# Performance work log

Measured on AMD Instinct MI355X. Metric: run time of the kernel, lower is better.

## Reference

```python
import jax, jax.numpy as jnp
import numpy as np

N_NODES = 50000
N_EDGES = 800000
DIM = 128
HEADS = 2
DEPTH = 2
MLP = 512
NEG_SLOPE = 0.2  # PyG GATv2 default
EPS = 1e-5


def setup_inputs() -> dict:
    key = jax.random.key(0)
    ks = jax.random.split(key, 10)
    s = 0.05
    p = lambda k, shape: (jax.random.normal(k, shape, jnp.float32) * s)
    x = jax.random.normal(ks[0], (N_NODES, DIM), jnp.float32)
    edge_index = jax.random.randint(ks[1], (2, N_EDGES), 0, N_NODES, dtype=jnp.int64)
    D, H = DEPTH, HEADS
    return {
        "x": x,
        "edge_index": edge_index,
        # per-layer stacked params (leading dim = depth)
        "ln1_g": jnp.ones((D, DIM), jnp.float32), "ln1_b": jnp.zeros((D, DIM), jnp.float32),
        "Wl": p(ks[2], (D, DIM, H * DIM)), "bl": jnp.zeros((D, H * DIM), jnp.float32),
        "Wr": p(ks[3], (D, DIM, H * DIM)), "br": jnp.zeros((D, H * DIM), jnp.float32),
        "att": p(ks[4], (D, H, DIM)),
        "gat_b": jnp.zeros((D, H * DIM), jnp.float32),
        "proj_W": p(ks[5], (D, H * DIM, DIM)), "proj_b": jnp.zeros((D, DIM), jnp.float32),
        "ln2_g": jnp.ones((D, DIM), jnp.float32), "ln2_b": jnp.zeros((D, DIM), jnp.float32),
        "W1": p(ks[6], (D, DIM, MLP)), "b1": jnp.zeros((D, MLP), jnp.float32),
        "W2": p(ks[7], (D, MLP, DIM)), "b2": jnp.zeros((D, DIM), jnp.float32),
    }


def _layer_norm(x, g, b):
    m = jnp.mean(x, axis=-1, keepdims=True)
    v = jnp.var(x, axis=-1, keepdims=True)
    return (x - m) * jax.lax.rsqrt(v + EPS) * g + b


def _gatv2(x, src, dst, Wl, bl, Wr, br, att, gat_b):
    # GATv2Conv: e_ij = att^T LeakyReLU(Wl x_j + Wr x_i); alpha = segment-softmax over dst
    n = x.shape[0]
    xl = (x @ Wl + bl).reshape(n, HEADS, DIM)  # source transform [N,H,D]
    xr = (x @ Wr + br).reshape(n, HEADS, DIM)  # target transform [N,H,D]
    e = jax.nn.leaky_relu(xl[src] + xr[dst], NEG_SLOPE)      # [E,H,D]
    score = jnp.einsum('ehd,hd->eh', e, att)                 # [E,H]
    smax = jax.ops.segment_max(score, dst, num_segments=n)   # [N,H]
    ex = jnp.exp(score - smax[dst])
    denom = jax.ops.segment_sum(ex, dst, num_segments=n)     # [N,H]
    alpha = ex / (denom[dst] + 1e-16)                        # [E,H]
    msg = xl[src] * alpha[..., None]                         # [E,H,D]
    out = jax.ops.segment_sum(msg, dst, num_segments=n)      # [N,H,D]
    return out.reshape(n, HEADS * DIM) + gat_b


def reference(x, edge_index, ln1_g, ln1_b, Wl, bl, Wr, br, att, gat_b,
              proj_W, proj_b, ln2_g, ln2_b, W1, b1, W2, b2):
    src, dst = edge_index[0], edge_index[1]
    for i in range(DEPTH):
        h = _layer_norm(x, ln1_g[i], ln1_b[i])               # PreNorm
        g = _gatv2(h, src, dst, Wl[i], bl[i], Wr[i], br[i], att[i], gat_b[i])
        x = x + (g @ proj_W[i] + proj_b[i])                  # QuickFix proj + Residual
        h = _layer_norm(x, ln2_g[i], ln2_b[i])
        x = x + (jax.nn.gelu(h @ W1[i] + b1[i]) @ W2[i] + b2[i])  # FFN + Residual
    return x
```

## Files before the change

### kernel.cpp

```cpp
#include <hip/hip_runtime.h>

typedef unsigned int uint;
typedef unsigned short ushort;
typedef __attribute__((ext_vector_type(4))) float f32x4;
typedef __attribute__((ext_vector_type(8))) short bf16x8;

#define N_NODES 50000
#define DIM 128
#define HEADS 2
#define HD 256
#define MLP 512
#define DEPTH 2
#define CAP 96

__device__ __forceinline__ float bf_lo(uint u) { return __uint_as_float(u << 16); }
__device__ __forceinline__ float bf_hi(uint u) { return __uint_as_float(u & 0xFFFF0000u); }
__device__ __forceinline__ uint f2bf(float f) {
    uint u = __float_as_uint(f);
    return (u + 0x7FFFu + ((u >> 16) & 1u)) >> 16;
}

__device__ __forceinline__ float gelu_tanh(float x) {
    float t = 0.7978845608028654f * (x + 0.044715f * x * x * x);
    float e = __expf(2.0f * t);
    float th = 1.0f - 2.0f / (e + 1.0f);
    return 0.5f * x * (1.0f + th);
}

__global__ __launch_bounds__(256) void ln_kernel(
    const float* __restrict__ x, const float* __restrict__ g,
    const float* __restrict__ b, ushort* __restrict__ out, int N)
{
    int node = blockIdx.x * 4 + (threadIdx.x >> 6);
    if (node >= N) return;
    int lane = threadIdx.x & 63;
    const float2 v = *(const float2*)(x + (size_t)node * DIM + lane * 2);
    float s = v.x + v.y;
    float s2 = v.x * v.x + v.y * v.y;
    #pragma unroll
    for (int m = 1; m <= 32; m <<= 1) {
        s  += __shfl_xor(s,  m, 64);
        s2 += __shfl_xor(s2, m, 64);
    }
    float mean = s * (1.0f / 128.0f);
    float var  = s2 * (1.0f / 128.0f) - mean * mean;
    float rs = rsqrtf(var + 1e-5f);
    float ox = (v.x - mean) * rs * g[lane * 2]     + b[lane * 2];
    float oy = (v.y - mean) * rs * g[lane * 2 + 1] + b[lane * 2 + 1];
    uint pk = f2bf(ox) | (f2bf(oy) << 16);
    *(uint*)(out + (size_t)node * DIM + lane * 2) = pk;
}

__global__ __launch_bounds__(256) void wconv_all(
    const float* __restrict__ Wl, const float* __restrict__ Wr,
    const float* __restrict__ pW, const float* __restrict__ W1,
    const float* __restrict__ W2, ushort* __restrict__ WlWr_t,
    ushort* __restrict__ pW_t, ushort* __restrict__ W1_t,
    ushort* __restrict__ W2_t)
{
    int i = blockIdx.x * 256 + threadIdx.x;
    if (i < 65536) {
        int l = i >> 15, rem = i & 32767;
        int k = rem >> 8, m = rem & 255;
        WlWr_t[l * 65536 + m * 128 + k] = (ushort)f2bf(Wl[i]);
    } else if (i < 131072) {
        int j = i - 65536;
        int l = j >> 15, rem = j & 32767;
        int k = rem >> 8, m = rem & 255;
        WlWr_t[l * 65536 + (m + 256) * 128 + k] = (ushort)f2bf(Wr[j]);
    } else if (i < 196608) {
        int j = i - 131072;
        int l = j >> 15, rem = j & 32767;
        int k = rem >> 7, m = rem & 127;
        pW_t[l * 32768 + m * 256 + k] = (ushort)f2bf(pW[j]);
    } else if (i < 327680) {
        int j = i - 196608;
        int l = j >> 16, rem = j & 65535;
        int k = rem >> 9, m = rem & 511;
        W1_t[l * 65536 + m * 128 + k] = (ushort)f2bf(W1[j]);
    } else if (i < 458752) {
        int j = i - 327680;
        int l = j >> 16, rem = j & 65535;
        int k = rem >> 7, m = rem & 127;
        W2_t[l * 65536 + m * 512 + k] = (ushort)f2bf(W2[j]);
    }
}

template<int EPI>
__global__ __launch_bounds__(256) void gemm_mfma(
    const ushort* __restrict__ A, const ushort* __restrict__ Bt,
    const float* __restrict__ bias, const float* __restrict__ bias2, int bsplit,
    const float* R, void* Cout, int Nr, int K, int M)
{
    __shared__ ushort As[128 * 72];
    __shared__ ushort Bs[64 * 72];
    const int tid = threadIdx.x;
    const int wave = tid >> 6, lane = tid & 63;
    const int wm = wave >> 1, wn = wave & 1;
    const int r0 = blockIdx.y * 128;
    const int c0 = blockIdx.x * 64;
    const int l15 = lane & 15, q = lane >> 4;

    f32x4 acc[4][2];
    #pragma unroll
    for (int t = 0; t < 4; ++t)
        #pragma unroll
        for (int u = 0; u < 2; ++u) {
            f32x4 z = {0.f, 0.f, 0.f, 0.f};
            acc[t][u] = z;
        }

    for (int k0 = 0; k0 < K; k0 += 64) {
        #pragma unroll
        for (int p = 0; p < 4; ++p) {
            int flat = p * 256 + tid;
            int row = flat >> 3, c8 = flat & 7;
            int gr = r0 + row; gr = gr < Nr ? gr : Nr - 1;
            uint4 v = *(const uint4*)(A + (size_t)gr * K + k0 + c8 * 8);
            *(uint4*)(As + row * 72 + c8 * 8) = v;
        }
        #pragma unroll
        for (int p = 0; p < 2; ++p) {
            int flat = p * 256 + tid;
            int row = flat >> 3, c8 = flat & 7;
            uint4 v = *(const uint4*)(Bt + (size_t)(c0 + row) * K + k0 + c8 * 8);
            *(uint4*)(Bs + row * 72 + c8 * 8) = v;
        }
        __syncthreads();
        #pragma unroll
        for (int kh = 0; kh < 2; ++kh) {
            const int ko = kh * 32 + q * 8;
            bf16x8 a[4], b[2];
            #pragma unroll
            for (int t = 0; t < 4; ++t)
                a[t] = *(const bf16x8*)(As + (wm * 64 + t * 16 + l15) * 72 + ko);
            #pragma unroll
            for (int u = 0; u < 2; ++u)
                b[u] = *(const bf16x8*)(Bs + (wn * 32 + u * 16 + l15) * 72 + ko);
            #pragma unroll
            for (int t = 0; t < 4; ++t)
                #pragma unroll
                for (int u = 0; u < 2; ++u)
                    acc[t][u] = __builtin_amdgcn_mfma_f32_16x16x32_bf16(
                        a[t], b[u], acc[t][u], 0, 0, 0);
        }
        __syncthreads();
    }

    #pragma unroll
    for (int t = 0; t < 4; ++t) {
        int grow = r0 + wm * 64 + t * 16 + q * 4;
        #pragma unroll
        for (int u = 0; u < 2; ++u) {
            int gcol = c0 + wn * 32 + u * 16 + l15;
            float bv = (gcol < bsplit) ? bias[gcol] : bias2[gcol - bsplit];
            #pragma unroll
            for (int i = 0; i < 4; ++i) {
                int r = grow + i;
                if (r >= Nr) continue;
                float v = acc[t][u][i] + bv;
                if (EPI == 1) v = gelu_tanh(v);
                if (EPI == 2) {
                    v += R[(size_t)r * M + gcol];
                    ((float*)Cout)[(size_t)r * M + gcol] = v;
                } else {
                    ((ushort*)Cout)[(size_t)r * M + gcol] = (ushort)f2bf(v);
                }
            }
        }
    }
}

__global__ __launch_bounds__(256) void bucket_kernel(
    const int* __restrict__ src, const int* __restrict__ dst,
    int* __restrict__ deg, int* __restrict__ esrc, int E)
{
    int e = blockIdx.x * 256 + threadIdx.x;
    if (e >= E) return;
    int d = dst[e];
    int pos = atomicAdd(&deg[d], 1);
    if (pos < CAP) esrc[(size_t)d * CAP + pos] = src[e];
}

__global__ __launch_bounds__(256) void gat_gather(
    const int* __restrict__ deg, const int* __restrict__ esrc,
    const ushort* __restrict__ xlr, const float* __restrict__ att,
    const float* __restrict__ gat_b, ushort* __restrict__ agg, int N)
{
    int node = blockIdx.x * 4 + (threadIdx.x >> 6);
    if (node >= N) return;
    const int lane = threadIdx.x & 63;
    const int half = lane >> 5, sl = lane & 31;
    const int c = sl * 8;

    const uint4 rq = *(const uint4*)(xlr + (size_t)node * 512 + 256 + c);
    const float r0 = bf_lo(rq.x), r1 = bf_hi(rq.x), r2 = bf_lo(rq.y), r3 = bf_hi(rq.y);
    const float r4 = bf_lo(rq.z), r5 = bf_hi(rq.z), r6 = bf_lo(rq.w), r7 = bf_hi(rq.w);
    const float4 a03 = *(const float4*)(att + c);
    const float4 a47 = *(const float4*)(att + c + 4);

    int dc = deg[node]; dc = dc < CAP ? dc : CAP;
    const int base = node * CAP;
    float acc0=0.f,acc1=0.f,acc2=0.f,acc3=0.f,acc4=0.f,acc5=0.f,acc6=0.f,acc7=0.f;
    float den = 0.f;

    for (int it = 0; it * 2 < dc; ++it) {
        const int e = it * 2 + half;
        const int idx = e < dc ? e : dc - 1;
        const int s = esrc[base + idx];
        const uint4 lq = *(const uint4*)(xlr + (size_t)s * 512 + c);
        const float l0 = bf_lo(lq.x), l1 = bf_hi(lq.x), l2 = bf_lo(lq.y), l3 = bf_hi(lq.y);
        const float l4 = bf_lo(lq.z), l5 = bf_hi(lq.z), l6 = bf_lo(lq.w), l7 = bf_hi(lq.w);
        float t, p = 0.f;
        t = l0 + r0; p += a03.x * fmaxf(t, 0.2f * t);
        t = l1 + r1; p += a03.y * fmaxf(t, 0.2f * t);
        t = l2 + r2; p += a03.z * fmaxf(t, 0.2f * t);
        t = l3 + r3; p += a03.w * fmaxf(t, 0.2f * t);
        t = l4 + r4; p += a47.x * fmaxf(t, 0.2f * t);
        t = l5 + r5; p += a47.y * fmaxf(t, 0.2f * t);
        t = l6 + r6; p += a47.z * fmaxf(t, 0.2f * t);
        t = l7 + r7; p += a47.w * fmaxf(t, 0.2f * t);
        p += __shfl_xor(p, 1, 64);
        p += __shfl_xor(p, 2, 64);
        p += __shfl_xor(p, 4, 64);
        p += __shfl_xor(p, 8, 64);
        const float ex = (e < dc) ? __expf(p) : 0.f;
        acc0 += ex * l0; acc1 += ex * l1; acc2 += ex * l2; acc3 += ex * l3;
        acc4 += ex * l4; acc5 += ex * l5; acc6 += ex * l6; acc7 += ex * l7;
        den += ex;
    }
    acc0 += __shfl_xor(acc0, 32, 64); acc1 += __shfl_xor(acc1, 32, 64);
    acc2 += __shfl_xor(acc2, 32, 64); acc3 += __shfl_xor(acc3, 32, 64);
    acc4 += __shfl_xor(acc4, 32, 64); acc5 += __shfl_xor(acc5, 32, 64);
    acc6 += __shfl_xor(acc6, 32, 64); acc7 += __shfl_xor(acc7, 32, 64);
    den  += __shfl_xor(den,  32, 64);

    if (half == 0) {
        const float inv = 1.0f / (den + 1e-16f);
        const float4 g03 = *(const float4*)(gat_b + c);
        const float4 g47 = *(const float4*)(gat_b + c + 4);
        uint4 o;
        o.x = f2bf(acc0 * inv + g03.x) | (f2bf(acc1 * inv + g03.y) << 16);
        o.y = f2bf(acc2 * inv + g03.z) | (f2bf(acc3 * inv + g03.w) << 16);
        o.z = f2bf(acc4 * inv + g47.x) | (f2bf(acc5 * inv + g47.y) << 16);
        o.w = f2bf(acc6 * inv + g47.z) | (f2bf(acc7 * inv + g47.w) << 16);
        *(uint4*)(agg + (size_t)node * HD + c) = o;
    }
}

extern "C" void kernel_launch(void* const* d_in, const int* in_sizes, int n_in,
                              void* d_out, int out_size, void* d_ws, size_t ws_size,
                              hipStream_t stream) {
    const float* x_in   = (const float*)d_in[0];
    const int*   eidx   = (const int*)d_in[1];
    const float* ln1_g  = (const float*)d_in[2];
    const float* ln1_b  = (const float*)d_in[3];
    const float* Wl     = (const float*)d_in[4];
    const float* bl     = (const float*)d_in[5];
    const float* Wr     = (const float*)d_in[6];
    const float* br     = (const float*)d_in[7];
    const float* att    = (const float*)d_in[8];
    const float* gat_b  = (const float*)d_in[9];
    const float* projW  = (const float*)d_in[10];
    const float* projb  = (const float*)d_in[11];
    const float* ln2_g  = (const float*)d_in[12];
    const float* ln2_b  = (const float*)d_in[13];
    const float* W1     = (const float*)d_in[14];
    const float* b1     = (const float*)d_in[15];
    const float* W2     = (const float*)d_in[16];
    const float* b2     = (const float*)d_in[17];

    const int N = N_NODES;
    const int E = in_sizes[1] / 2;
    const int* src = eidx;
    const int* dst = eidx + E;

    char* ws = (char*)d_ws;
    size_t off = 0;
    ushort* xlr  = (ushort*)(ws + off); off += (size_t)N * 512 * 2;
    ushort* agg  = (ushort*)(ws + off); off += (size_t)N * HD * 2;
    ushort* h    = (ushort*)(ws + off); off += (size_t)N * DIM * 2;
    ushort* WlWr_t = (ushort*)(ws + off); off += (size_t)DEPTH * 512 * 128 * 2;
    ushort* pW_t   = (ushort*)(ws + off); off += (size_t)DEPTH * 128 * 256 * 2;
    ushort* W1_t   = (ushort*)(ws + off); off += (size_t)DEPTH * 512 * 128 * 2;
    ushort* W2_t   = (ushort*)(ws + off); off += (size_t)DEPTH * 128 * 512 * 2;
    int* deg     = (int*)(ws + off);    off += (size_t)N * 4;
    int* esrc    = (int*)(ws + off);    off += (size_t)N * CAP * 4;
    ushort* mid  = xlr;

    float* x = (float*)d_out;
    hipMemcpyAsync(x, x_in, (size_t)N * DIM * 4, hipMemcpyDeviceToDevice, stream);

    const int nodeBlocks = (N + 3) / 4;
    const dim3 blk(256);
    const int gy = (N + 127) / 128;
    const float* nullb = nullptr;

    wconv_all<<<(458752 + 255) / 256, blk, 0, stream>>>(
        Wl, Wr, projW, W1, W2, WlWr_t, pW_t, W1_t, W2_t);

    hipMemsetAsync(deg, 0, (size_t)N * 4, stream);
    bucket_kernel<<<(E + 255) / 256, blk, 0, stream>>>(src, dst, deg, esrc, E);

    for (int L = 0; L < DEPTH; ++L) {
        const float* bl_i   = bl + (size_t)L * HD;
        const float* br_i   = br + (size_t)L * HD;
        const float* att_i  = att + (size_t)L * HD;
        const float* gatb_i = gat_b + (size_t)L * HD;
        const float* pb_i   = projb + (size_t)L * DIM;
        const float* b1_i   = b1 + (size_t)L * MLP;
        const float* b2_i   = b2 + (size_t)L * DIM;

        ln_kernel<<<nodeBlocks, blk, 0, stream>>>(x, ln1_g + L * DIM, ln1_b + L * DIM, h, N);
        gemm_mfma<0><<<dim3(512 / 64, gy), blk, 0, stream>>>(
            h, WlWr_t + (size_t)L * 512 * 128, bl_i, br_i, HD, nullptr, xlr, N, DIM, 512);
        gat_gather<<<nodeBlocks, blk, 0, stream>>>(deg, esrc, xlr, att_i, gatb_i, agg, N);
        gemm_mfma<2><<<dim3(DIM / 64, gy), blk, 0, stream>>>(
            agg, pW_t + (size_t)L * 128 * 256, pb_i, pb_i, 1 << 30, x, x, N, HD, DIM);
        ln_kernel<<<nodeBlocks, blk, 0, stream>>>(x, ln2_g + L * DIM, ln2_b + L * DIM, h, N);
        gemm_mfma<1><<<dim3(MLP / 64, gy), blk, 0, stream>>>(
            h, W1_t + (size_t)L * 512 * 128, b1_i, b1_i, 1 << 30, nullptr, mid, N, DIM, MLP);
        gemm_mfma<2><<<dim3(DIM / 64, gy), blk, 0, stream>>>(
            mid, W2_t + (size_t)L * 128 * 512, b2_i, b2_i, 1 << 30, x, x, N, MLP, DIM);
    }
}
```

Baseline: 598.9 us.

## Replace LDS-staged GEMM with direct-from-global MFMA loads and larger wave tiles

The shared-memory staged GEMM becomes a kernel in which each wave loads its A and B fragments straight from global memory into registers. There are no LDS buffers and no barriers. Each wave now computes a 64x64 tile (block 128x128), K is a template parameter, and occupancy is hinted via launch bounds. This removes LDS round trips and syncs, but relies on L1/L2 for the data reuse that LDS used to provide. It also raises register pressure and issues strided global loads.

```diff
diff --git a/kernel.cpp b/kernel.cpp
--- a/kernel.cpp
+++ b/kernel.cpp
@@ -86,73 +86,62 @@
     }
 }
 
-template<int EPI>
-__global__ __launch_bounds__(256) void gemm_mfma(
+template<int K, int EPI>
+__global__ __launch_bounds__(256, 4) void gemm_direct(
     const ushort* __restrict__ A, const ushort* __restrict__ Bt,
     const float* __restrict__ bias, const float* __restrict__ bias2, int bsplit,
-    const float* R, void* Cout, int Nr, int K, int M)
-{
-    __shared__ ushort As[128 * 72];
-    __shared__ ushort Bs[64 * 72];
+    const float* __restrict__ R, void* __restrict__ Cout, int Nr, int M)
+{
     const int tid = threadIdx.x;
     const int wave = tid >> 6, lane = tid & 63;
     const int wm = wave >> 1, wn = wave & 1;
-    const int r0 = blockIdx.y * 128;
-    const int c0 = blockIdx.x * 64;
+    const int r0 = blockIdx.y * 128 + wm * 64;
+    const int c0 = blockIdx.x * 128 + wn * 64;
     const int l15 = lane & 15, q = lane >> 4;
 
-    f32x4 acc[4][2];
+    const ushort* Arow[4];
+    const ushort* Brow[4];
+    #pragma unroll
+    for (int t = 0; t < 4; ++t) {
+        int r = r0 + t * 16 + l15; r = r < Nr ? r : Nr - 1;
+        Arow[t] = A + (size_t)r * K + q * 8;
+        Brow[t] = Bt + (size_t)(c0 + t * 16 + l15) * K + q * 8;
+    }
+
+    f32x4 acc[4][4];
     #pragma unroll
     for (int t = 0; t < 4; ++t)
         #pragma unroll
-        for (int u = 0; u < 2; ++u) {
+        for (int u = 0; u < 4; ++u) {
             f32x4 z = {0.f, 0.f, 0.f, 0.f};
             acc[t][u] = z;
         }
 
-    for (int k0 = 0; k0 < K; k0 += 64) {
+    #pragma unroll 1
+    for (int kb = 0; kb < K / 128; ++kb) {
         #pragma unroll
-        for (int p = 0; p < 4; ++p) {
-            int flat = p * 256 + tid;
-            int row = flat >> 3, c8 = flat & 7;
-            int gr = r0 + row; gr = gr < Nr ? gr : Nr - 1;
-            uint4 v = *(const uint4*)(A + (size_t)gr * K + k0 + c8 * 8);
-            *(uint4*)(As + row * 72 + c8 * 8) = v;
-        }
-        #pragma unroll
-        for (int p = 0; p < 2; ++p) {
-            int flat = p * 256 + tid;
-            int row = flat >> 3, c8 = flat & 7;
-            uint4 v = *(const uint4*)(Bt + (size_t)(c0 + row) * K + k0 + c8 * 8);
-            *(uint4*)(Bs + row * 72 + c8 * 8) = v;
-        }
-        __syncthreads();
-        #pragma unroll
-        for (int kh = 0; kh < 2; ++kh) {
-            const int ko = kh * 32 + q * 8;
-            bf16x8 a[4], b[2];
+        for (int kh = 0; kh < 4; ++kh) {
+            const int ko = kb * 128 + kh * 32;
+            bf16x8 a[4], b[4];
             #pragma unroll
-            for (int t = 0; t < 4; ++t)
-                a[t] = *(const bf16x8*)(As + (wm * 64 + t * 16 + l15) * 72 + ko);
+            for (int t = 0; t < 4; ++t) a[t] = *(const bf16x8*)(Arow[t] + ko);
             #pragma unroll
-            for (int u = 0; u < 2; ++u)
-                b[u] = *(const bf16x8*)(Bs + (wn * 32 + u * 16 + l15) * 72 + ko);
+            for (int u = 0; u < 4; ++u) b[u] = *(const bf16x8*)(Brow[u] + ko);
             #pragma unroll
             for (int t = 0; t < 4; ++t)
                 #pragma unroll
-                for (int u = 0; u < 2; ++u)
+                for (int u = 0; u < 4; ++u)
                     acc[t][u] = __builtin_amdgcn_mfma_f32_16x16x32_bf16(
                         a[t], b[u], acc[t][u], 0, 0, 0);
         }
-        __syncthreads();
     }
 
     #pragma unroll
     for (int t = 0; t < 4; ++t) {
-        int grow = r0 + wm * 64 + t * 16 + q * 4;
+        int grow = r0 + t * 16 + q * 4;
         #pragma unroll
-        for (int u = 0; u < 2; ++u) {
-            int gcol = c0 + wn * 32 + u * 16 + l15;
+        for (int u = 0; u < 4; ++u) {
+            int gcol = c0 + u * 16 + l15;
             float bv = (gcol < bsplit) ? bias[gcol] : bias2[gcol - bsplit];
             #pragma unroll
             for (int i = 0; i < 4; ++i) {
@@ -294,7 +283,6 @@
     const int nodeBlocks = (N + 3) / 4;
     const dim3 blk(256);
     const int gy = (N + 127) / 128;
-    const float* nullb = nullptr;
 
     wconv_all<<<(458752 + 255) / 256, blk, 0, stream>>>(
         Wl, Wr, projW, W1, W2, WlWr_t, pW_t, W1_t, W2_t);
@@ -312,15 +300,15 @@
         const float* b2_i   = b2 + (size_t)L * DIM;
 
         ln_kernel<<<nodeBlocks, blk, 0, stream>>>(x, ln1_g + L * DIM, ln1_b + L * DIM, h, N);
-        gemm_mfma<0><<<dim3(512 / 64, gy), blk, 0, stream>>>(
-            h, WlWr_t + (size_t)L * 512 * 128, bl_i, br_i, HD, nullptr, xlr, N, DIM, 512);
+        gemm_direct<128, 0><<<dim3(4, gy), blk, 0, stream>>>(
+            h, WlWr_t + (size_t)L * 512 * 128, bl_i, br_i, HD, nullptr, xlr, N, 512);
         gat_gather<<<nodeBlocks, blk, 0, stream>>>(deg, esrc, xlr, att_i, gatb_i, agg, N);
-        gemm_mfma<2><<<dim3(DIM / 64, gy), blk, 0, stream>>>(
-            agg, pW_t + (size_t)L * 128 * 256, pb_i, pb_i, 1 << 30, x, x, N, HD, DIM);
+        gemm_direct<256, 2><<<dim3(1, gy), blk, 0, stream>>>(
+            agg, pW_t + (size_t)L * 128 * 256, pb_i, pb_i, 1 << 30, x, x, N, DIM);
         ln_kernel<<<nodeBlocks, blk, 0, stream>>>(x, ln2_g + L * DIM, ln2_b + L * DIM, h, N);
-        gemm_mfma<1><<<dim3(MLP / 64, gy), blk, 0, stream>>>(
-            h, W1_t + (size_t)L * 512 * 128, b1_i, b1_i, 1 << 30, nullptr, mid, N, DIM, MLP);
-        gemm_mfma<2><<<dim3(DIM / 64, gy), blk, 0, stream>>>(
-            mid, W2_t + (size_t)L * 128 * 512, b2_i, b2_i, 1 << 30, x, x, N, MLP, DIM);
-    }
-}
+        gemm_direct<128, 1><<<dim3(4, gy), blk, 0, stream>>>(
+            h, W1_t + (size_t)L * 512 * 128, b1_i, b1_i, 1 << 30, nullptr, mid, N, 512);
+        gemm_direct<512, 2><<<dim3(1, gy), blk, 0, stream>>>(
+            mid, W2_t + (size_t)L * 128 * 512, b2_i, b2_i, 1 << 30, x, x, N, DIM);
+    }
+}
```

Result: slower. 716.4 us (+19.6%).

## Widen GEMM tile to 128x128 and pack gather math into float2 vectors

Applied to the files above, without the earlier changes.

The MFMA GEMM block tile grows from 128x64 to 128x128, so each wave computes a 64x64 sub-tile with 16 accumulators. That halves the number of column blocks and the repeated loads of the A tile. The GAT gather kernel now holds pairs in float2 vectors, which may let the compiler use packed FP32 instructions. The larger tile raises register and LDS use, which can lower occupancy, and the N=128 GEMMs drop to one column block per row tile, reducing parallelism.

```diff
diff --git a/kernel.cpp b/kernel.cpp
--- a/kernel.cpp
+++ b/kernel.cpp
@@ -3,6 +3,7 @@
 typedef unsigned int uint;
 typedef unsigned short ushort;
 typedef __attribute__((ext_vector_type(4))) float f32x4;
+typedef __attribute__((ext_vector_type(2))) float f32x2;
 typedef __attribute__((ext_vector_type(8))) short bf16x8;
 
 #define N_NODES 50000
@@ -13,11 +14,15 @@
 #define DEPTH 2
 #define CAP 96
 
-__device__ __forceinline__ float bf_lo(uint u) { return __uint_as_float(u << 16); }
-__device__ __forceinline__ float bf_hi(uint u) { return __uint_as_float(u & 0xFFFF0000u); }
 __device__ __forceinline__ uint f2bf(float f) {
     uint u = __float_as_uint(f);
     return (u + 0x7FFFu + ((u >> 16) & 1u)) >> 16;
+}
+__device__ __forceinline__ f32x2 bfpair(uint u) {
+    f32x2 r;
+    r.x = __uint_as_float(u << 16);
+    r.y = __uint_as_float(u & 0xFFFF0000u);
+    return r;
 }
 
 __device__ __forceinline__ float gelu_tanh(float x) {
@@ -93,19 +98,19 @@
     const float* R, void* Cout, int Nr, int K, int M)
 {
     __shared__ ushort As[128 * 72];
-    __shared__ ushort Bs[64 * 72];
+    __shared__ ushort Bs[128 * 72];
     const int tid = threadIdx.x;
     const int wave = tid >> 6, lane = tid & 63;
     const int wm = wave >> 1, wn = wave & 1;
     const int r0 = blockIdx.y * 128;
-    const int c0 = blockIdx.x * 64;
+    const int c0 = blockIdx.x * 128;
     const int l15 = lane & 15, q = lane >> 4;
 
-    f32x4 acc[4][2];
+    f32x4 acc[4][4];
     #pragma unroll
     for (int t = 0; t < 4; ++t)
         #pragma unroll
-        for (int u = 0; u < 2; ++u) {
+        for (int u = 0; u < 4; ++u) {
             f32x4 z = {0.f, 0.f, 0.f, 0.f};
             acc[t][u] = z;
         }
@@ -120,7 +125,7 @@
             *(uint4*)(As + row * 72 + c8 * 8) = v;
         }
         #pragma unroll
-        for (int p = 0; p < 2; ++p) {
+        for (int p = 0; p < 4; ++p) {
             int flat = p * 256 + tid;
             int row = flat >> 3, c8 = flat & 7;
             uint4 v = *(const uint4*)(Bt + (size_t)(c0 + row) * K + k0 + c8 * 8);
@@ -130,17 +135,17 @@
         #pragma unroll
         for (int kh = 0; kh < 2; ++kh) {
             const int ko = kh * 32 + q * 8;
-            bf16x8 a[4], b[2];
+            bf16x8 a[4], b[4];
             #pragma unroll
             for (int t = 0; t < 4; ++t)
                 a[t] = *(const bf16x8*)(As + (wm * 64 + t * 16 + l15) * 72 + ko);
             #pragma unroll
-            for (int u = 0; u < 2; ++u)
-                b[u] = *(const bf16x8*)(Bs + (wn * 32 + u * 16 + l15) * 72 + ko);
+            for (int u = 0; u < 4; ++u)
+                b[u] = *(const bf16x8*)(Bs + (wn * 64 + u * 16 + l15) * 72 + ko);
             #pragma unroll
             for (int t = 0; t < 4; ++t)
                 #pragma unroll
-                for (int u = 0; u < 2; ++u)
+                for (int u = 0; u < 4; ++u)
                     acc[t][u] = __builtin_amdgcn_mfma_f32_16x16x32_bf16(
                         a[t], b[u], acc[t][u], 0, 0, 0);
         }
@@ -151,8 +156,8 @@
     for (int t = 0; t < 4; ++t) {
         int grow = r0 + wm * 64 + t * 16 + q * 4;
         #pragma unroll
-        for (int u = 0; u < 2; ++u) {
-            int gcol = c0 + wn * 32 + u * 16 + l15;
+        for (int u = 0; u < 4; ++u) {
+            int gcol = c0 + wn * 64 + u * 16 + l15;
             float bv = (gcol < bsplit) ? bias[gcol] : bias2[gcol - bsplit];
             #pragma unroll
             for (int i = 0; i < 4; ++i) {
@@ -194,14 +199,16 @@
     const int c = sl * 8;
 
     const uint4 rq = *(const uint4*)(xlr + (size_t)node * 512 + 256 + c);
-    const float r0 = bf_lo(rq.x), r1 = bf_hi(rq.x), r2 = bf_lo(rq.y), r3 = bf_hi(rq.y);
-    const float r4 = bf_lo(rq.z), r5 = bf_hi(rq.z), r6 = bf_lo(rq.w), r7 = bf_hi(rq.w);
-    const float4 a03 = *(const float4*)(att + c);
-    const float4 a47 = *(const float4*)(att + c + 4);
+    const f32x2 r01 = bfpair(rq.x), r23 = bfpair(rq.y);
+    const f32x2 r45 = bfpair(rq.z), r67 = bfpair(rq.w);
+    const float4 af0 = *(const float4*)(att + c);
+    const float4 af1 = *(const float4*)(att + c + 4);
+    const f32x2 a01 = {af0.x, af0.y}, a23 = {af0.z, af0.w};
+    const f32x2 a45 = {af1.x, af1.y}, a67 = {af1.z, af1.w};
 
     int dc = deg[node]; dc = dc < CAP ? dc : CAP;
     const int base = node * CAP;
-    float acc0=0.f,acc1=0.f,acc2=0.f,acc3=0.f,acc4=0.f,acc5=0.f,acc6=0.f,acc7=0.f;
+    f32x2 acc01 = {0.f, 0.f}, acc23 = {0.f, 0.f}, acc45 = {0.f, 0.f}, acc67 = {0.f, 0.f};
     float den = 0.f;
 
     for (int it = 0; it * 2 < dc; ++it) {
@@ -209,41 +216,37 @@
         const int idx = e < dc ? e : dc - 1;
         const int s = esrc[base + idx];
         const uint4 lq = *(const uint4*)(xlr + (size_t)s * 512 + c);
-        const float l0 = bf_lo(lq.x), l1 = bf_hi(lq.x), l2 = bf_lo(lq.y), l3 = bf_hi(lq.y);
-        const float l4 = bf_lo(lq.z), l5 = bf_hi(lq.z), l6 = bf_lo(lq.w), l7 = bf_hi(lq.w);
-        float t, p = 0.f;
-        t = l0 + r0; p += a03.x * fmaxf(t, 0.2f * t);
-        t = l1 + r1; p += a03.y * fmaxf(t, 0.2f * t);
-        t = l2 + r2; p += a03.z * fmaxf(t, 0.2f * t);
-        t = l3 + r3; p += a03.w * fmaxf(t, 0.2f * t);
-        t = l4 + r4; p += a47.x * fmaxf(t, 0.2f * t);
-        t = l5 + r5; p += a47.y * fmaxf(t, 0.2f * t);
-        t = l6 + r6; p += a47.z * fmaxf(t, 0.2f * t);
-        t = l7 + r7; p += a47.w * fmaxf(t, 0.2f * t);
+        const f32x2 l01 = bfpair(lq.x), l23 = bfpair(lq.y);
+        const f32x2 l45 = bfpair(lq.z), l67 = bfpair(lq.w);
+        f32x2 t, p2;
+        t = l01 + r01; p2  = a01 * __builtin_elementwise_max(t, 0.2f * t);
+        t = l23 + r23; p2 += a23 * __builtin_elementwise_max(t, 0.2f * t);
+        t = l45 + r45; p2 += a45 * __builtin_elementwise_max(t, 0.2f * t);
+        t = l67 + r67; p2 += a67 * __builtin_elementwise_max(t, 0.2f * t);
+        float p = p2.x + p2.y;
         p += __shfl_xor(p, 1, 64);
         p += __shfl_xor(p, 2, 64);
         p += __shfl_xor(p, 4, 64);
         p += __shfl_xor(p, 8, 64);
         const float ex = (e < dc) ? __expf(p) : 0.f;
-        acc0 += ex * l0; acc1 += ex * l1; acc2 += ex * l2; acc3 += ex * l3;
-        acc4 += ex * l4; acc5 += ex * l5; acc6 += ex * l6; acc7 += ex * l7;
+        acc01 += ex * l01; acc23 += ex * l23; acc45 += ex * l45; acc67 += ex * l67;
         den += ex;
     }
-    acc0 += __shfl_xor(acc0, 32, 64); acc1 += __shfl_xor(acc1, 32, 64);
-    acc2 += __shfl_xor(acc2, 32, 64); acc3 += __shfl_xor(acc3, 32, 64);
-    acc4 += __shfl_xor(acc4, 32, 64); acc5 += __shfl_xor(acc5, 32, 64);
-    acc6 += __shfl_xor(acc6, 32, 64); acc7 += __shfl_xor(acc7, 32, 64);
-    den  += __shfl_xor(den,  32, 64);
+    acc01.x += __shfl_xor(acc01.x, 32, 64); acc01.y += __shfl_xor(acc01.y, 32, 64);
+    acc23.x += __shfl_xor(acc23.x, 32, 64); acc23.y += __shfl_xor(acc23.y, 32, 64);
+    acc45.x += __shfl_xor(acc45.x, 32, 64); acc45.y += __shfl_xor(acc45.y, 32, 64);
+    acc67.x += __shfl_xor(acc67.x, 32, 64); acc67.y += __shfl_xor(acc67.y, 32, 64);
+    den     += __shfl_xor(den,     32, 64);
 
     if (half == 0) {
         const float inv = 1.0f / (den + 1e-16f);
-        const float4 g03 = *(const float4*)(gat_b + c);
-        const float4 g47 = *(const float4*)(gat_b + c + 4);
+        const float4 g0 = *(const float4*)(gat_b + c);
+        const float4 g1 = *(const float4*)(gat_b + c + 4);
         uint4 o;
-        o.x = f2bf(acc0 * inv + g03.x) | (f2bf(acc1 * inv + g03.y) << 16);
-        o.y = f2bf(acc2 * inv + g03.z) | (f2bf(acc3 * inv + g03.w) << 16);
-        o.z = f2bf(acc4 * inv + g47.x) | (f2bf(acc5 * inv + g47.y) << 16);
-        o.w = f2bf(acc6 * inv + g47.z) | (f2bf(acc7 * inv + g47.w) << 16);
+        o.x = f2bf(acc01.x * inv + g0.x) | (f2bf(acc01.y * inv + g0.y) << 16);
+        o.y = f2bf(acc23.x * inv + g0.z) | (f2bf(acc23.y * inv + g0.w) << 16);
+        o.z = f2bf(acc45.x * inv + g1.x) | (f2bf(acc45.y * inv + g1.y) << 16);
+        o.w = f2bf(acc67.x * inv + g1.z) | (f2bf(acc67.y * inv + g1.w) << 16);
         *(uint4*)(agg + (size_t)node * HD + c) = o;
     }
 }
@@ -294,7 +297,6 @@
     const int nodeBlocks = (N + 3) / 4;
     const dim3 blk(256);
     const int gy = (N + 127) / 128;
-    const float* nullb = nullptr;
 
     wconv_all<<<(458752 + 255) / 256, blk, 0, stream>>>(
         Wl, Wr, projW, W1, W2, WlWr_t, pW_t, W1_t, W2_t);
@@ -312,15 +314,15 @@
         const float* b2_i   = b2 + (size_t)L * DIM;
 
         ln_kernel<<<nodeBlocks, blk, 0, stream>>>(x, ln1_g + L * DIM, ln1_b + L * DIM, h, N);
-        gemm_mfma<0><<<dim3(512 / 64, gy), blk, 0, stream>>>(
-            h, WlWr_t + (size_t)L * 512 * 128, bl_i, br_i, HD, nullptr, xlr, N, DIM, 512);
+        gemm_mfma<0><<<dim3(4, gy), blk, 0, stream>>>(
+            h, WlWr_t + (size_t)L * 512 * 128, bl_i, br_i, HD, nullptr, xlr, N, 128, 512);
         gat_gather<<<nodeBlocks, blk, 0, stream>>>(deg, esrc, xlr, att_i, gatb_i, agg, N);
-        gemm_mfma<2><<<dim3(DIM / 64, gy), blk, 0, stream>>>(
-            agg, pW_t + (size_t)L * 128 * 256, pb_i, pb_i, 1 << 30, x, x, N, HD, DIM);
+        gemm_mfma<2><<<dim3(1, gy), blk, 0, stream>>>(
+            agg, pW_t + (size_t)L * 128 * 256, pb_i, pb_i, 1 << 30, x, x, N, 256, 128);
         ln_kernel<<<nodeBlocks, blk, 0, stream>>>(x, ln2_g + L * DIM, ln2_b + L * DIM, h, N);
-        gemm_mfma<1><<<dim3(MLP / 64, gy), blk, 0, stream>>>(
-            h, W1_t + (size_t)L * 512 * 128, b1_i, b1_i, 1 << 30, nullptr, mid, N, DIM, MLP);
-        gemm_mfma<2><<<dim3(DIM / 64, gy), blk, 0, stream>>>(
-            mid, W2_t + (size_t)L * 128 * 512, b2_i, b2_i, 1 << 30, x, x, N, MLP, DIM);
-    }
-}
+        gemm_mfma<1><<<dim3(4, gy), blk, 0, stream>>>(
+            h, W1_t + (size_t)L * 512 * 128, b1_i, b1_i, 1 << 30, nullptr, mid, N, 128, 512);
+        gemm_mfma<2><<<dim3(1, gy), blk, 0, stream>>>(
+            mid, W2_t + (size_t)L * 128 * 512, b2_i, b2_i, 1 << 30, x, x, N, 512, 128);
+    }
+}
```

Result: slower. 651.4 us (+8.8%).
